# Performance work log

Measured on AMD Instinct MI355X. Metric: run time of the kernel, lower is better.

Reference implementation:

```python
import jax, jax.numpy as jnp
import numpy as np

POOL = 7  # pool_size


def setup_inputs() -> dict:
    key = jax.random.key(0)
    k1, k2, k3, k4, k5 = jax.random.split(key, 5)
    H = W = 64
    C = 1024
    R = 1024  # num_rois
    img = jax.random.normal(k1, (1, H, W, C), dtype=jnp.float32)
    x = jax.random.randint(k2, (1, R), 0, W - 16)
    y = jax.random.randint(k3, (1, R), 0, H - 16)
    w = jax.random.randint(k4, (1, R), 1, 17)
    h = jax.random.randint(k5, (1, R), 1, 17)
    rois = jnp.stack([x, y, w, h], axis=-1).astype(jnp.int32)  # (1, R, 4)
    return {"img": img, "rois": rois}


def _axis_coords(start, size, pool):
    """Per-ROI bilinear source coords for tf.image.resize (half-pixel centers).
    start,size: (R,) int32. Returns absolute low/high indices (R,pool) int32
    and interpolation weight (R,pool) float32."""
    scale = size.astype(jnp.float32) / pool
    src = (jnp.arange(pool, dtype=jnp.float32) + 0.5)[None, :] * scale[:, None] - 0.5
    f = jnp.floor(src)
    lerp = src - f
    lo = jnp.clip(f.astype(jnp.int32), 0, size[:, None] - 1)
    hi = jnp.clip(f.astype(jnp.int32) + 1, 0, size[:, None] - 1)
    return start[:, None] + lo, start[:, None] + hi, lerp


def reference(img, rois):
    # img: (1, H, W, C); rois: (1, R, 4) int32 with (x, y, w, h)
    r = rois[0]
    x, y, w, h = r[:, 0], r[:, 1], r[:, 2], r[:, 3]
    y0, y1, ty = _axis_coords(y, h, POOL)  # (R, P)
    x0, x1, tx = _axis_coords(x, w, POOL)  # (R, P)
    im = img[0]  # (H, W, C)

    def gather(yy, xx):
        # (R, P, P, C) corner gather, vectorized over all ROIs
        return im[yy[:, :, None], xx[:, None, :], :]

    tx_ = tx[:, None, :, None]
    ty_ = ty[:, :, None, None]
    top = gather(y0, x0) * (1.0 - tx_) + gather(y0, x1) * tx_
    bot = gather(y1, x0) * (1.0 - tx_) + gather(y1, x1) * tx_
    out = top * (1.0 - ty_) + bot * ty_  # (R, P, P, C)
    return out[None]  # (1, R, P, P, C)
```

## Files before the change

### kernel.cpp

```cpp
#include <hip/hip_runtime.h>


#define POOLSZ 7
#define IMG_H 64
#define IMG_W 64
#define IMG_C 1024
#define NUM_XCD 8

typedef float v4f __attribute__((ext_vector_type(4)));

__device__ __forceinline__ int src_y0(int ry, int rh, int py) {
    const float scy  = (float)rh * (1.0f / (float)POOLSZ);
    const float srcy = ((float)py + 0.5f) * scy - 0.5f;
    const int   iy   = (int)floorf(srcy);
    return ry + min(max(iy, 0), rh - 1);
}

__global__ __launch_bounds__(256) void row_sort_kernel(
    const int* __restrict__ rois, int* __restrict__ order, int R) {
    __shared__ int cnt[64];
    __shared__ int ofs[64];
    const int t = threadIdx.x;
    const int n = R * POOLSZ;
    if (t < 64) cnt[t] = 0;
    __syncthreads();
    for (int i = t; i < n; i += 256) {
        const int r  = i / POOLSZ;
        const int py = i - r * POOLSZ;
        const int y0 = src_y0(rois[r * 4 + 1], rois[r * 4 + 3], py) & 63;
        atomicAdd(&cnt[y0], 1);
    }
    __syncthreads();
    if (t == 0) {
        int s = 0;
        for (int i = 0; i < 64; ++i) { ofs[i] = s; s += cnt[i]; }
    }
    __syncthreads();
    for (int i = t; i < n; i += 256) {
        const int r  = i / POOLSZ;
        const int py = i - r * POOLSZ;
        const int y0 = src_y0(rois[r * 4 + 1], rois[r * 4 + 3], py) & 63;
        const int p  = atomicAdd(&ofs[y0], 1);
        order[p] = i;
    }
}

__global__ __launch_bounds__(256, 4) void roi_pool_row_kernel(
    const float* __restrict__ img,
    const int* __restrict__ rois,
    float* __restrict__ out,
    int rowsPerXcd,
    const int* __restrict__ order) {
    int rowIdx;
    if (rowsPerXcd > 0) {
        const int xcd   = blockIdx.x & (NUM_XCD - 1);
        const int local = blockIdx.x >> 3;
        rowIdx = xcd * rowsPerXcd + local;
    } else {
        rowIdx = blockIdx.x;
    }
    const int rid = order ? order[rowIdx] : rowIdx;
    const int r  = rid / POOLSZ;
    const int py = rid - r * POOLSZ;

    const int4 roi = ((const int4*)rois)[r];
    const int rx = roi.x, ry = roi.y, rw = roi.z, rh = roi.w;

    const float scy  = (float)rh * (1.0f / (float)POOLSZ);
    const float srcy = ((float)py + 0.5f) * scy - 0.5f;
    const float fy   = floorf(srcy);
    const float ty   = srcy - fy;
    const int   iy   = (int)fy;
    const int   y0   = ry + min(max(iy,     0), rh - 1);
    const int   y1   = ry + min(max(iy + 1, 0), rh - 1);

    const int c4 = threadIdx.x;
    const v4f* __restrict__ base = (const v4f*)img + c4;
    const int rb0 = y0 * (IMG_W * IMG_C / 4);
    const int rb1 = y1 * (IMG_W * IMG_C / 4);

    v4f* __restrict__ dst =
        (v4f*)out + ((size_t)r * POOLSZ + py) * POOLSZ * (IMG_C / 4) + c4;

    const float scx = (float)rw * (1.0f / (float)POOLSZ);
#pragma unroll
    for (int px = 0; px < POOLSZ; ++px) {
        const float srcx = ((float)px + 0.5f) * scx - 0.5f;
        const float fx   = floorf(srcx);
        const float tx   = srcx - fx;
        const int   ix   = (int)fx;
        const int   xo0  = (rx + min(max(ix,     0), rw - 1)) * (IMG_C / 4);
        const int   xo1  = (rx + min(max(ix + 1, 0), rw - 1)) * (IMG_C / 4);

        const v4f a = base[rb0 + xo0];
        const v4f b = base[rb0 + xo1];
        const v4f c = base[rb1 + xo0];
        const v4f d = base[rb1 + xo1];

        const v4f top = a + (b - a) * tx;
        const v4f bot = c + (d - c) * tx;
        dst[px * (IMG_C / 4)] = top + (bot - top) * ty;
    }
}

extern "C" void kernel_launch(void* const* d_in, const int* in_sizes, int n_in,
                              void* d_out, int out_size, void* d_ws, size_t ws_size,
                              hipStream_t stream) {
    const float* img  = (const float*)d_in[0];
    const int*   rois = (const int*)d_in[1];
    float*       out  = (float*)d_out;
    const int R = in_sizes[1] / 4;
    const int n_rows = R * POOLSZ;
    const int rowsPerXcd = (n_rows % NUM_XCD == 0) ? (n_rows / NUM_XCD) : 0;

    int* order = nullptr;
    if (ws_size >= (size_t)n_rows * sizeof(int)) {
        order = (int*)d_ws;
        row_sort_kernel<<<1, 256, 0, stream>>>(rois, order, R);
    }
    roi_pool_row_kernel<<<n_rows, 256, 0, stream>>>(img, rois, out, rowsPerXcd, order);
}
```

Baseline: 260.5 us.

## Stage two image rows per y-bin in LDS and process all rows in bin

The row-sort kernel now also records bin start offsets. A new kernel launches one block per (source row bin, channel split). Each block loads image rows y0 and y0+1 for its channel slice into shared memory and then interpolates every output row whose y0 falls in that bin, so corner gathers come from LDS instead of global or L2. The trade-offs are a grid of only 512 blocks, uneven work across bins, a 64 KB LDS footprint that limits occupancy, and loss of the XCD-aware mapping.

```diff
diff --git a/kernel.cpp b/kernel.cpp
--- a/kernel.cpp
+++ b/kernel.cpp
@@ -6,6 +6,9 @@
 #define IMG_W 64
 #define IMG_C 1024
 #define NUM_XCD 8
+#define SPLITS 8
+#define CH_V4 (IMG_C / 4)
+#define SPLIT_V4 (CH_V4 / SPLITS)
 
 typedef float v4f __attribute__((ext_vector_type(4)));
 
@@ -17,7 +20,8 @@
 }
 
 __global__ __launch_bounds__(256) void row_sort_kernel(
-    const int* __restrict__ rois, int* __restrict__ order, int R) {
+    const int* __restrict__ rois, int* __restrict__ order,
+    int* __restrict__ binStart, int R) {
     __shared__ int cnt[64];
     __shared__ int ofs[64];
     const int t = threadIdx.x;
@@ -33,7 +37,8 @@
     __syncthreads();
     if (t == 0) {
         int s = 0;
-        for (int i = 0; i < 64; ++i) { ofs[i] = s; s += cnt[i]; }
+        for (int i = 0; i < 64; ++i) { ofs[i] = s; binStart[i] = s; s += cnt[i]; }
+        binStart[64] = s;
     }
     __syncthreads();
     for (int i = t; i < n; i += 256) {
@@ -45,23 +50,85 @@
     }
 }
 
+__global__ __launch_bounds__(256, 2) void roi_pool_bin_kernel(
+    const float* __restrict__ img,
+    const int* __restrict__ rois,
+    float* __restrict__ out,
+    const int* __restrict__ order,
+    const int* __restrict__ binStart) {
+    const int bin   = blockIdx.x >> 3;
+    const int split = blockIdx.x & (SPLITS - 1);
+    const int start = binStart[bin];
+    const int cnt   = binStart[bin + 1] - start;
+    if (cnt == 0) return;
+
+    __shared__ v4f lds[2 * IMG_W * SPLIT_V4];
+    const int t = threadIdx.x;
+    {
+        const v4f* __restrict__ img4 = (const v4f*)img;
+        const int y_hi = min(bin + 1, IMG_H - 1);
+#pragma unroll
+        for (int k = 0; k < 16; ++k) {
+            const int j   = t + k * 256;
+            const int row = j >> 11;
+            const int rem = j & 2047;
+            const int x   = rem >> 5;
+            const int c4  = rem & 31;
+            const int y   = row ? y_hi : bin;
+            lds[j] = img4[((size_t)(y * IMG_W + x)) * CH_V4 + split * SPLIT_V4 + c4];
+        }
+    }
+    __syncthreads();
+
+    const int grp  = t >> 5;
+    const int lane = t & 31;
+    v4f* __restrict__ out4 = (v4f*)out;
+
+    for (int row = grp; row < cnt; row += 8) {
+        const int rid = order[start + row];
+        const int r   = rid / POOLSZ;
+        const int py  = rid - r * POOLSZ;
+        const int4 roi = ((const int4*)rois)[r];
+        const int rx = roi.x, ry = roi.y, rw = roi.z, rh = roi.w;
+
+        const float scy  = (float)rh * (1.0f / (float)POOLSZ);
+        const float srcy = ((float)py + 0.5f) * scy - 0.5f;
+        const float fy   = floorf(srcy);
+        const float ty   = srcy - fy;
+        const int   iy   = (int)fy;
+        const int y1 = ry + min(max(iy + 1, 0), rh - 1);
+        const int l1 = (y1 - bin) << 11;
+
+        const float scx = (float)rw * (1.0f / (float)POOLSZ);
+        const size_t obase = (size_t)rid * (POOLSZ * CH_V4) + split * SPLIT_V4 + lane;
+#pragma unroll
+        for (int px = 0; px < POOLSZ; ++px) {
+            const float srcx = ((float)px + 0.5f) * scx - 0.5f;
+            const float fx   = floorf(srcx);
+            const float tx   = srcx - fx;
+            const int   ix   = (int)fx;
+            const int xo0 = (rx + min(max(ix,     0), rw - 1)) << 5;
+            const int xo1 = (rx + min(max(ix + 1, 0), rw - 1)) << 5;
+
+            const v4f a = lds[xo0 + lane];
+            const v4f b = lds[xo1 + lane];
+            const v4f c = lds[l1 + xo0 + lane];
+            const v4f d = lds[l1 + xo1 + lane];
+
+            const v4f top = a + (b - a) * tx;
+            const v4f bot = c + (d - c) * tx;
+            out4[obase + (size_t)px * CH_V4] = top + (bot - top) * ty;
+        }
+    }
+}
+
 __global__ __launch_bounds__(256, 4) void roi_pool_row_kernel(
     const float* __restrict__ img,
     const int* __restrict__ rois,
-    float* __restrict__ out,
-    int rowsPerXcd,
-    const int* __restrict__ order) {
-    int rowIdx;
-    if (rowsPerXcd > 0) {
-        const int xcd   = blockIdx.x & (NUM_XCD - 1);
-        const int local = blockIdx.x >> 3;
-        rowIdx = xcd * rowsPerXcd + local;
-    } else {
-        rowIdx = blockIdx.x;
-    }
-    const int rid = order ? order[rowIdx] : rowIdx;
-    const int r  = rid / POOLSZ;
-    const int py = rid - r * POOLSZ;
+    float* __restrict__ out) {
+    const int rowIdx = blockIdx.x;
+    const int r  = rowIdx / POOLSZ;
+    const int py = rowIdx - r * POOLSZ;
 
     const int4 roi = ((const int4*)rois)[r];
     const int rx = roi.x, ry = roi.y, rw = roi.z, rh = roi.w;
@@ -76,11 +143,10 @@
 
     const int c4 = threadIdx.x;
     const v4f* __restrict__ base = (const v4f*)img + c4;
-    const int rb0 = y0 * (IMG_W * IMG_C / 4);
-    const int rb1 = y1 * (IMG_W * IMG_C / 4);
-
+    const int rb0 = y0 * (IMG_W * CH_V4);
+    const int rb1 = y1 * (IMG_W * CH_V4);
     v4f* __restrict__ dst =
-        (v4f*)out + ((size_t)r * POOLSZ + py) * POOLSZ * (IMG_C / 4) + c4;
+        (v4f*)out + ((size_t)r * POOLSZ + py) * POOLSZ * CH_V4 + c4;
 
     const float scx = (float)rw * (1.0f / (float)POOLSZ);
 #pragma unroll
@@ -89,8 +155,8 @@
         const float fx   = floorf(srcx);
         const float tx   = srcx - fx;
         const int   ix   = (int)fx;
-        const int   xo0  = (rx + min(max(ix,     0), rw - 1)) * (IMG_C / 4);
-        const int   xo1  = (rx + min(max(ix + 1, 0), rw - 1)) * (IMG_C / 4);
+        const int   xo0  = (rx + min(max(ix,     0), rw - 1)) * CH_V4;
+        const int   xo1  = (rx + min(max(ix + 1, 0), rw - 1)) * CH_V4;
 
         const v4f a = base[rb0 + xo0];
         const v4f b = base[rb0 + xo1];
@@ -99,7 +165,7 @@
 
         const v4f top = a + (b - a) * tx;
         const v4f bot = c + (d - c) * tx;
-        dst[px * (IMG_C / 4)] = top + (bot - top) * ty;
+        dst[px * CH_V4] = top + (bot - top) * ty;
     }
 }
 
@@ -111,12 +177,15 @@
     float*       out  = (float*)d_out;
     const int R = in_sizes[1] / 4;
     const int n_rows = R * POOLSZ;
-    const int rowsPerXcd = (n_rows % NUM_XCD == 0) ? (n_rows / NUM_XCD) : 0;
 
-    int* order = nullptr;
-    if (ws_size >= (size_t)n_rows * sizeof(int)) {
-        order = (int*)d_ws;
-        row_sort_kernel<<<1, 256, 0, stream>>>(rois, order, R);
+    const size_t ws_need = (size_t)(n_rows + 65) * sizeof(int);
+    if (ws_size >= ws_need) {
+        int* order    = (int*)d_ws;
+        int* binStart = order + n_rows;
+        row_sort_kernel<<<1, 256, 0, stream>>>(rois, order, binStart, R);
+        roi_pool_bin_kernel<<<64 * SPLITS, 256, 0, stream>>>(
+            img, rois, out, order, binStart);
+    } else {
+        roi_pool_row_kernel<<<n_rows, 256, 0, stream>>>(img, rois, out);
     }
-    roi_pool_row_kernel<<<n_rows, 256, 0, stream>>>(img, rois, out, rowsPerXcd, order);
 }
```

Result: faster. 236.1 us (-9.4%).
